# Optimization experiments

Measured on AMD Instinct MI355X. Metric: run time of the kernel, lower is better.

## Reference

```python
import jax, jax.numpy as jnp
import numpy as np

HEADS = 8
DK = 64            # key_size == size_per_head
NEIGHBORS = 3
KSIZE = 1 + 2 * NEIGHBORS  # 7 (rate=1)


def setup_inputs() -> dict:
    key = jax.random.key(0)
    k1, k2, k3, k4 = jax.random.split(key, 4)
    B, HW, S, D = 2, 64, 256, 512
    inputs = jax.random.normal(k1, (B, HW, S, D), dtype=jnp.float32)
    pos_bias = jax.random.normal(k2, (HEADS, S, KSIZE), dtype=jnp.float32)
    W_qkv = jax.random.normal(k3, (D, 3 * HEADS * DK), dtype=jnp.float32) * 0.02
    W_out = jax.random.normal(k4, (HEADS * DK, D), dtype=jnp.float32) * 0.02
    return {"inputs": inputs, "pos_bias": pos_bias, "W_qkv": W_qkv, "W_out": W_out}


def reference(inputs, pos_bias, W_qkv, W_out):
    B, HW, S, D = inputs.shape
    # qkv projection (no bias), split into q, k, v
    qkv = inputs @ W_qkv                                   # [B,HW,S,3*H*DK]
    q, k, v = jnp.split(qkv, 3, axis=-1)
    q = (q / jnp.sqrt(jnp.float32(DK))).reshape(B, HW, S, HEADS, DK)
    k = k.reshape(B, HW, S, HEADS, DK)
    v = v.reshape(B, HW, S, HEADS, DK)

    # zero-pad keys/values along seq (faithful to F.pad with value=0)
    pad = NEIGHBORS
    kp = jnp.pad(k, ((0, 0), (0, 0), (pad, pad), (0, 0), (0, 0)))
    vp = jnp.pad(v, ((0, 0), (0, 0), (pad, pad), (0, 0), (0, 0)))

    # sliding-window gather: window w for query i covers padded positions i..i+KSIZE-1
    idx = jnp.arange(S)[:, None] + jnp.arange(KSIZE)[None, :]  # [S,KSIZE]
    kw = kp[:, :, idx]                                         # [B,HW,S,KSIZE,H,DK]
    vw = vp[:, :, idx]                                         # [B,HW,S,KSIZE,H,DK]

    # scores over the window
    attn = jnp.einsum('bnshd,bnswhd->bnswh', q, kw)            # [B,HW,S,KSIZE,H]
    # additive positional bias: [H,S,KSIZE] -> [S,KSIZE,H] broadcast
    attn = attn + jnp.transpose(pos_bias, (1, 2, 0))[None, None]
    attn = jax.nn.softmax(attn, axis=-2)                       # softmax over window dim

    out = jnp.einsum('bnswh,bnswhd->bnshd', attn, vw)          # [B,HW,S,H,DK]
    out = out.reshape(B, HW, S, HEADS * DK)
    return out @ W_out
```

## Files before the change

kernel.cpp:

```cpp
#include <hip/hip_runtime.h>
#include <hip/hip_bf16.h>
#include <cstdint>


typedef __bf16 bf16x8 __attribute__((ext_vector_type(8)));
typedef float f32x4 __attribute__((ext_vector_type(4)));

__device__ __forceinline__ uint16_t f2bf(float f) {
    uint32_t u = __builtin_bit_cast(uint32_t, f);
    return (uint16_t)((u + 0x7fffu + ((u >> 16) & 1u)) >> 16);
}
__device__ __forceinline__ float bflo(uint32_t u) { return __builtin_bit_cast(float, u << 16); }
__device__ __forceinline__ float bfhi(uint32_t u) { return __builtin_bit_cast(float, u & 0xffff0000u); }

__device__ __forceinline__ void unpack8(uint4 v, float* f) {
    f[0] = bflo(v.x); f[1] = bfhi(v.x);
    f[2] = bflo(v.y); f[3] = bfhi(v.y);
    f[4] = bflo(v.z); f[5] = bfhi(v.z);
    f[6] = bflo(v.w); f[7] = bfhi(v.w);
}
__device__ __forceinline__ uint32_t pack2(float a, float b) {
    return (uint32_t)f2bf(a) | ((uint32_t)f2bf(b) << 16);
}

#define GLOAD_LDS16(gp, lp)                                                        \
    __builtin_amdgcn_global_load_lds((const __attribute__((address_space(1))) void*)(gp), \
                                     (__attribute__((address_space(3))) void*)(lp), 16, 0, 0)

__device__ __forceinline__ bf16x8 ds_read16(const uint16_t* p) {
    bf16x8 r;
    asm volatile("ds_read_b128 %0, %1"
                 : "=v"(r)
                 : "v"((const __attribute__((address_space(3))) void*)p));
    return r;
}

__global__ void prep(const float* __restrict__ X, const float* __restrict__ Wqkv,
                     const float* __restrict__ Wout, uint16_t* __restrict__ Xb,
                     uint16_t* __restrict__ WqkvT, uint16_t* __restrict__ WoutT) {
    int b = blockIdx.x;
    if (b < 8192) {
        int i = b * 256 + threadIdx.x;
        const float4* p = (const float4*)X + (size_t)i * 2;
        float4 a = p[0], q = p[1];
        uint4 o;
        o.x = pack2(a.x, a.y);
        o.y = pack2(a.z, a.w);
        o.z = pack2(q.x, q.y);
        o.w = pack2(q.z, q.w);
        *((uint4*)Xb + i) = o;
    } else {
        int idx = (b - 8192) * 256 + threadIdx.x;
        if (idx < 512 * 1536) {
            int r = idx / 1536, c = idx - r * 1536;
            WqkvT[(size_t)c * 512 + r] = f2bf(Wqkv[idx]);
        } else {
            idx -= 512 * 1536;
            int r = idx >> 9, c = idx & 511;
            WoutT[(size_t)c * 512 + r] = f2bf(Wout[idx]);
        }
    }
}

__global__ __launch_bounds__(512, 2)
void gemm_qkv_attn(const uint16_t* __restrict__ Xb, const uint16_t* __restrict__ WqkvT,
                   const float* __restrict__ pb, uint16_t* __restrict__ attn) {
    __shared__ __align__(16) uint16_t lds[57344];

    constexpr int KO = 16384;
    constexpr int VO = 33152;
    constexpr int PO = 49920;

    const int tid  = threadIdx.x;
    const int lane = tid & 63;
    const int wv   = tid >> 6;
    const int r    = lane & 15;
    const int quad = lane >> 4;
    const int wr   = wv >> 1;
    const int wc   = wv & 1;
    const int h    = blockIdx.x >> 7;
    const int bn   = blockIdx.x & 127;
    const long bm0 = (long)bn * 256;

    const uint16_t* srcp[4];
    int rel[4];
#pragma unroll
    for (int i = 0; i < 4; ++i) {
        int j = wv * 256 + i * 64 + lane;
        if (j < 1024) {
            int d = j, ln = d >> 3, pre = (d & 7) ^ (ln & 7);
            int row = 2 * ln + (pre >> 2), col = (pre & 3) * 8;
            srcp[i] = Xb + (bm0 + row) * 512L + col;
            rel[i]  = d * 8;
        } else {
            int e = j - 1024, ln = e >> 3, pre = (e & 7) ^ (ln & 7);
            int row = 2 * ln + (pre >> 2), col = (pre & 3) * 8;
            long grow = ((long)(row >> 6)) * 512 + h * 64 + (row & 63);
            srcp[i] = WqkvT + grow * 512 + col;
            rel[i]  = e * 8;
        }
    }

#define STAGE(q_, t_) do {                                                              \
        if (wv < 4) {                                                                   \
            _Pragma("unroll")                                                           \
            for (int i_ = 0; i_ < 4; ++i_)                                              \
                GLOAD_LDS16(srcp[i_] + (t_) * 32, &lds[(q_) * 8192 + rel[i_]]);         \
        } else if (wv < 7) {                                                            \
            _Pragma("unroll")                                                           \
            for (int i_ = 0; i_ < 4; ++i_)                                              \
                GLOAD_LDS16(srcp[i_] + (t_) * 32, &lds[32768 + (q_) * 6144 + rel[i_]]); \
        }                                                                               \
    } while (0)

    const int p_ln  = (((r & 1) << 2) | quad) ^ ((r >> 1) & 7);
    const int aLane = wr * 2048 + (r >> 1) * 64 + p_ln * 8;
    const int bLane = wc * 3072 + (r >> 1) * 64 + p_ln * 8;

    f32x4 acc[4][6];
#pragma unroll
    for (int mf = 0; mf < 4; ++mf)
#pragma unroll
        for (int nf = 0; nf < 6; ++nf) acc[mf][nf] = (f32x4){0.f, 0.f, 0.f, 0.f};

    bf16x8 fA0[4], fB0[6], fA1[4], fB1[6];

#define READS(q_, FA_, FB_) do {                                                        \
        const int ao_ = (q_) * 8192, bo_ = 32768 + (q_) * 6144;                         \
        _Pragma("unroll")                                                               \
        for (int nf_ = 0; nf_ < 6; ++nf_) FB_[nf_] = ds_read16(&lds[bo_ + bLane + nf_ * 512]); \
        _Pragma("unroll")                                                               \
        for (int mf_ = 0; mf_ < 4; ++mf_) FA_[mf_] = ds_read16(&lds[ao_ + aLane + mf_ * 512]); \
    } while (0)

#define BODY(t_, FAn_, FBn_, FAc_, FBc_) do {                                           \
        if ((t_) + 1 < 16) {                                                            \
            READS(((t_) + 1) & 3, FAn_, FBn_);                                          \
            asm volatile("s_waitcnt lgkmcnt(10)" ::: "memory");                         \
        } else {                                                                        \
            asm volatile("s_waitcnt lgkmcnt(0)" ::: "memory");                          \
        }                                                                               \
        __builtin_amdgcn_sched_barrier(0);                                              \
        __builtin_amdgcn_s_setprio(1);                                                  \
        _Pragma("unroll")                                                               \
        for (int nf_ = 0; nf_ < 6; ++nf_)                                               \
            _Pragma("unroll")                                                           \
            for (int mf_ = 0; mf_ < 4; ++mf_)                                           \
                acc[mf_][nf_] = __builtin_amdgcn_mfma_f32_16x16x32_bf16(                \
                    FBc_[nf_], FAc_[mf_], acc[mf_][nf_], 0, 0, 0);                      \
        __builtin_amdgcn_s_setprio(0);                                                  \
        if ((t_) + 3 < 16) {                                                            \
            STAGE(((t_) + 3) & 3, (t_) + 3);                                            \
            asm volatile("s_waitcnt vmcnt(4)" ::: "memory");                            \
        } else {                                                                        \
            asm volatile("s_waitcnt vmcnt(0)" ::: "memory");                            \
        }                                                                               \
        if ((t_) < 15) __builtin_amdgcn_s_barrier();                                    \
    } while (0)

    STAGE(0, 0);
    STAGE(1, 1);
    STAGE(2, 2);
    asm volatile("s_waitcnt vmcnt(4)" ::: "memory");
    __builtin_amdgcn_s_barrier();
    READS(0, fA0, fB0);

    for (int tt = 0; tt < 16; tt += 2) {
        BODY(tt,     fA1, fB1, fA0, fB0);
        BODY(tt + 1, fA0, fB0, fA1, fB1);
    }

    asm volatile("s_waitcnt vmcnt(0) lgkmcnt(0)" ::: "memory");
    __builtin_amdgcn_s_barrier();

    if (tid < 96) {
        int a    = tid / 48;
        int rem  = tid - a * 48;
        int hr6  = rem >> 3;
        int c8   = rem & 7;
        int hrow = (hr6 < 3) ? hr6 : (256 + hr6);
        ((uint4*)&lds[a ? VO : KO])[hrow * 8 + c8] = (uint4){0u, 0u, 0u, 0u};
    }

#pragma unroll
    for (int nf = 0; nf < 6; ++nf) {
        int arr, d0;
        if (wc == 0) { if (nf < 4) { arr = 0; d0 = nf * 16; } else { arr = 1; d0 = (nf - 4) * 16; } }
        else         { if (nf < 2) { arr = 1; d0 = 32 + nf * 16; } else { arr = 2; d0 = (nf - 2) * 16; } }
        const int base = (arr == 0) ? 0 : ((arr == 1) ? KO : VO);
        const int hofs = (arr == 0) ? 0 : 3;
        const int cc0  = (d0 >> 3) + (quad >> 1);
        const int sub  = (quad & 1) * 4;
#pragma unroll
        for (int mf = 0; mf < 4; ++mf) {
            int rowX = wr * 64 + mf * 16 + r + hofs;
            uint2 w;
            w.x = pack2(acc[mf][nf][0], acc[mf][nf][1]);
            w.y = pack2(acc[mf][nf][2], acc[mf][nf][3]);
            *(uint2*)&lds[base + rowX * 64 + ((cc0 ^ (rowX & 7)) << 3) + sub] = w;
        }
    }
    __syncthreads();

    const int s     = tid & 255;
    const int half  = tid >> 8;
    const int cbase = half * 4;
    float* pp = (float*)&lds[PO];

    uint4 qc[4];
    const uint4* qarr = (const uint4*)lds;
#pragma unroll
    for (int c = 0; c < 4; ++c) qc[c] = qarr[s * 8 + ((cbase + c) ^ (s & 7))];

    float sc[7];
#pragma unroll
    for (int w = 0; w < 7; ++w) sc[w] = 0.f;
    const uint4* karr = (const uint4*)&lds[KO];
#pragma unroll
    for (int c = 0; c < 4; ++c) {
        float qf[8];
        unpack8(qc[c], qf);
#pragma unroll
        for (int w = 0; w < 7; ++w) {
            int hrow = s + w;
            uint4 kc = karr[hrow * 8 + ((cbase + c) ^ (hrow & 7))];
            float kf[8];
            unpack8(kc, kf);
#pragma unroll
            for (int j = 0; j < 8; ++j) sc[w] += qf[j] * kf[j];
        }
    }

    if (half == 1) {
#pragma unroll
        for (int w = 0; w < 7; ++w) pp[s * 8 + w] = sc[w];
    }
    __syncthreads();

    if (half == 0) {
        const float* pbr = pb + ((size_t)h * 256 + s) * 7;
        float mx = -1e30f, tot[7];
#pragma unroll
        for (int w = 0; w < 7; ++w) {
            tot[w] = (sc[w] + pp[s * 8 + w]) * 0.125f + pbr[w];
            mx = fmaxf(mx, tot[w]);
        }
        float sum = 0.f;
#pragma unroll
        for (int w = 0; w < 7; ++w) {
            tot[w] = __expf(tot[w] - mx);
            sum += tot[w];
        }
        const float inv = 1.f / sum;
#pragma unroll
        for (int w = 0; w < 7; ++w) pp[s * 8 + w] = tot[w] * inv;
    }
    __syncthreads();

    float p[7];
#pragma unroll
    for (int w = 0; w < 7; ++w) p[w] = pp[s * 8 + w];

    const uint4* varr = (const uint4*)&lds[VO];
    uint4 ov[4];
#pragma unroll
    for (int c = 0; c < 4; ++c) {
        float o[8] = {0.f, 0.f, 0.f, 0.f, 0.f, 0.f, 0.f, 0.f};
#pragma unroll
        for (int w = 0; w < 7; ++w) {
            int hrow = s + w;
            uint4 vc = varr[hrow * 8 + ((cbase + c) ^ (hrow & 7))];
            float vf[8];
            unpack8(vc, vf);
#pragma unroll
            for (int j = 0; j < 8; ++j) o[j] += p[w] * vf[j];
        }
        ov[c].x = pack2(o[0], o[1]);
        ov[c].y = pack2(o[2], o[3]);
        ov[c].z = pack2(o[4], o[5]);
        ov[c].w = pack2(o[6], o[7]);
    }
    uint16_t* orow = attn + ((size_t)(bn * 256 + s)) * 512 + h * 64 + cbase * 8;
#pragma unroll
    for (int c = 0; c < 4; ++c) *(uint4*)(orow + c * 8) = ov[c];
#undef STAGE
#undef READS
#undef BODY
}

template <bool F32OUT>
__global__ __launch_bounds__(512, 4)
void gemm_mn(const uint16_t* __restrict__ A, const uint16_t* __restrict__ BT,
             void* __restrict__ Cout, int M, int N, int K) {
    __shared__ __align__(16) uint16_t lds[36864];

    const int tid  = threadIdx.x;
    const int lane = tid & 63;
    const int wv   = tid >> 6;
    const int r    = lane & 15;
    const int quad = lane >> 4;
    const int wr   = wv >> 1;
    const int wc   = wv & 1;
    const long bm0 = (long)blockIdx.x * 256;
    const long bn0 = (long)blockIdx.y * 128;
    const int NT   = K >> 5;

#define SRC_ROWCOL(d_, row_, col_) do {                                                 \
        int ln_ = (d_) >> 3, pre_ = ((d_) & 7) ^ (ln_ & 7);                             \
        row_ = 2 * ln_ + (pre_ >> 2);                                                   \
        col_ = (pre_ & 3) * 8;                                                          \
    } while (0)
    int rA0, cA0, rA1, cA1, rB0, cB0;
    SRC_ROWCOL(tid,       rA0, cA0);
    SRC_ROWCOL(tid + 512, rA1, cA1);
    SRC_ROWCOL(tid,       rB0, cB0);
    const uint16_t* pA0 = A  + (bm0 + rA0) * (long)K + cA0;
    const uint16_t* pA1 = A  + (bm0 + rA1) * (long)K + cA1;
    const uint16_t* pB0 = BT + (bn0 + rB0) * (long)K + cB0;
#undef SRC_ROWCOL

#define STAGE(b_, t_) do {                                                              \
        GLOAD_LDS16(pA0 + (t_) * 32, &lds[(b_) * 8192 + tid * 8]);                      \
        GLOAD_LDS16(pA1 + (t_) * 32, &lds[(b_) * 8192 + (tid + 512) * 8]);              \
        GLOAD_LDS16(pB0 + (t_) * 32, &lds[24576 + (b_) * 4096 + tid * 8]);              \
    } while (0)

    const int p_ln  = (((r & 1) << 2) | quad) ^ ((r >> 1) & 7);
    const int aLane = wr * 2048 + (r >> 1) * 64 + p_ln * 8;
    const int bLane = 24576 + wc * 2048 + (r >> 1) * 64 + p_ln * 8;

#define DS_A(mf_) ds_read16(&lds[aoff + aLane + (mf_) * 512])
#define DS_B(nf_) ds_read16(&lds[boff + bLane + (nf_) * 512])
#define WAITK2 do { asm volatile("s_waitcnt lgkmcnt(2)" ::: "memory");                  \
                    __builtin_amdgcn_sched_barrier(0); } while (0)
#define WAITK0 do { asm volatile("s_waitcnt lgkmcnt(0)" ::: "memory");                  \
                    __builtin_amdgcn_sched_barrier(0); } while (0)
#define MFMA_CL(m0_, f0_, f1_)                                                          \
    __builtin_amdgcn_s_setprio(1);                                                      \
    _Pragma("unroll")                                                                   \
    for (int nf = 0; nf < 4; ++nf)                                                      \
        acc[(m0_)][nf] = __builtin_amdgcn_mfma_f32_16x16x32_bf16(bfr[nf], f0_,          \
                                                                 acc[(m0_)][nf], 0, 0, 0); \
    _Pragma("unroll")                                                                   \
    for (int nf = 0; nf < 4; ++nf)                                                      \
        acc[(m0_) + 1][nf] = __builtin_amdgcn_mfma_f32_16x16x32_bf16(bfr[nf], f1_,      \
                                                                 acc[(m0_) + 1][nf], 0, 0, 0); \
    __builtin_amdgcn_s_setprio(0);

    f32x4 acc[4][4];
#pragma unroll
    for (int mf = 0; mf < 4; ++mf)
#pragma unroll
        for (int nf = 0; nf < 4; ++nf) acc[mf][nf] = (f32x4){0.f, 0.f, 0.f, 0.f};

    STAGE(0, 0);
    STAGE(1, 1);
    asm volatile("s_waitcnt vmcnt(3)" ::: "memory");
    __builtin_amdgcn_s_barrier();

    int b = 0, bs = 2;
    for (int t = 0; t < NT; ++t) {
        const int aoff = b * 8192;
        const int boff = b * 4096;

        if (t + 2 < NT) STAGE(bs, t + 2);

        bf16x8 bfr[4], a0, a1, a2, a3;
#pragma unroll
        for (int nf = 0; nf < 4; ++nf) bfr[nf] = DS_B(nf);
        a0 = DS_A(0); a1 = DS_A(1);
        a2 = DS_A(2); a3 = DS_A(3);

        WAITK2;
        MFMA_CL(0, a0, a1)
        WAITK0;
        MFMA_CL(2, a2, a3)

        if (t + 1 < NT) {
            if (t + 2 < NT)
                asm volatile("s_waitcnt vmcnt(3)" ::: "memory");
            else
                asm volatile("s_waitcnt vmcnt(0)" ::: "memory");
            __builtin_amdgcn_s_barrier();
        }
        b  = (b  == 2) ? 0 : b + 1;
        bs = (bs == 2) ? 0 : bs + 1;
    }

#pragma unroll
    for (int mf = 0; mf < 4; ++mf) {
        long m = bm0 + wr * 64 + mf * 16 + r;
#pragma unroll
        for (int nf = 0; nf < 4; ++nf) {
            long n0 = bn0 + wc * 64 + nf * 16 + quad * 4;
            if (F32OUT) {
                float4 v = {acc[mf][nf][0], acc[mf][nf][1], acc[mf][nf][2], acc[mf][nf][3]};
                *(float4*)((float*)Cout + m * (long)N + n0) = v;
            } else {
                uint2 w;
                w.x = pack2(acc[mf][nf][0], acc[mf][nf][1]);
                w.y = pack2(acc[mf][nf][2], acc[mf][nf][3]);
                *(uint2*)((uint16_t*)Cout + m * (long)N + n0) = w;
            }
        }
    }
#undef STAGE
#undef DS_A
#undef DS_B
#undef WAITK2
#undef WAITK0
#undef MFMA_CL
}

extern "C" void kernel_launch(void* const* d_in, const int* in_sizes, int n_in,
                              void* d_out, int out_size, void* d_ws, size_t ws_size,
                              hipStream_t stream) {
    const float* X    = (const float*)d_in[0];
    const float* pb   = (const float*)d_in[1];
    const float* Wqkv = (const float*)d_in[2];
    const float* Wout = (const float*)d_in[3];
    float* out = (float*)d_out;

    char* ws = (char*)d_ws;
    uint16_t* WqkvT = (uint16_t*)(ws);
    uint16_t* WoutT = (uint16_t*)(ws + 1572864);
    uint16_t* Xb    = (uint16_t*)(ws + 2097152);
    uint16_t* attnb = (uint16_t*)(ws + 35651584);

    prep<<<12288, 256, 0, stream>>>(X, Wqkv, Wout, Xb, WqkvT, WoutT);
    gemm_qkv_attn<<<1024, 512, 0, stream>>>(Xb, WqkvT, pb, attnb);
    gemm_mn<true><<<dim3(128, 4), 512, 0, stream>>>(attnb, WoutT, out, 32768, 512, 512);
}
```

Before: 230.7 us.

## Fuse fp32-to-bf16 conversion of X into the QKV GEMM load path

Drops the separate prep pass that converted X to bf16 in workspace. The QKV+attention kernel now loads fp32 X directly with register loads, packs it to bf16 and writes it into swizzled LDS, while the weights still go through direct global-to-LDS loads. The main pipeline goes from a 4-deep LDS ring to double buffering with full vmcnt/lgkmcnt waits and a barrier every step. This removes the conversion kernel's X write and re-read, but each head's block now reads twice as many bytes of X, and latency hiding in the main loop is shallower.

Result: slower. 241.1 us (+4.5%).

```diff
diff --git a/kernel.cpp b/kernel.cpp
--- a/kernel.cpp
+++ b/kernel.cpp
@@ -5,6 +5,7 @@
 
 typedef __bf16 bf16x8 __attribute__((ext_vector_type(8)));
 typedef float f32x4 __attribute__((ext_vector_type(4)));
+typedef uint32_t u32x4 __attribute__((ext_vector_type(4)));
 
 __device__ __forceinline__ uint16_t f2bf(float f) {
     uint32_t u = __builtin_bit_cast(uint32_t, f);
@@ -34,42 +35,41 @@
                  : "v"((const __attribute__((address_space(3))) void*)p));
     return r;
 }
-
-__global__ void prep(const float* __restrict__ X, const float* __restrict__ Wqkv,
-                     const float* __restrict__ Wout, uint16_t* __restrict__ Xb,
+__device__ __forceinline__ void ds_write16(uint16_t* p, u32x4 w) {
+    asm volatile("ds_write_b128 %0, %1"
+                 :: "v"((__attribute__((address_space(3))) void*)p), "v"(w)
+                 : "memory");
+}
+__device__ __forceinline__ f32x4 gload4f(const float* p) {
+    f32x4 r;
+    asm volatile("global_load_dwordx4 %0, %1, off"
+                 : "=v"(r)
+                 : "v"((const __attribute__((address_space(1))) void*)p));
+    return r;
+}
+
+__global__ void prep(const float* __restrict__ Wqkv, const float* __restrict__ Wout,
                      uint16_t* __restrict__ WqkvT, uint16_t* __restrict__ WoutT) {
-    int b = blockIdx.x;
-    if (b < 8192) {
-        int i = b * 256 + threadIdx.x;
-        const float4* p = (const float4*)X + (size_t)i * 2;
-        float4 a = p[0], q = p[1];
-        uint4 o;
-        o.x = pack2(a.x, a.y);
-        o.y = pack2(a.z, a.w);
-        o.z = pack2(q.x, q.y);
-        o.w = pack2(q.z, q.w);
-        *((uint4*)Xb + i) = o;
+    int idx = blockIdx.x * 256 + threadIdx.x;
+    if (idx < 512 * 1536) {
+        int r = idx / 1536, c = idx - r * 1536;
+        WqkvT[(size_t)c * 512 + r] = f2bf(Wqkv[idx]);
     } else {
-        int idx = (b - 8192) * 256 + threadIdx.x;
-        if (idx < 512 * 1536) {
-            int r = idx / 1536, c = idx - r * 1536;
-            WqkvT[(size_t)c * 512 + r] = f2bf(Wqkv[idx]);
-        } else {
-            idx -= 512 * 1536;
-            int r = idx >> 9, c = idx & 511;
-            WoutT[(size_t)c * 512 + r] = f2bf(Wout[idx]);
-        }
+        idx -= 512 * 1536;
+        int r = idx >> 9, c = idx & 511;
+        WoutT[(size_t)c * 512 + r] = f2bf(Wout[idx]);
     }
 }
 
 __global__ __launch_bounds__(512, 2)
-void gemm_qkv_attn(const uint16_t* __restrict__ Xb, const uint16_t* __restrict__ WqkvT,
+void gemm_qkv_attn(const float* __restrict__ X, const uint16_t* __restrict__ WqkvT,
                    const float* __restrict__ pb, uint16_t* __restrict__ attn) {
-    __shared__ __align__(16) uint16_t lds[57344];
+    __shared__ __align__(16) uint16_t lds[54016];
 
     constexpr int KO = 16384;
     constexpr int VO = 33152;
     constexpr int PO = 49920;
+    constexpr int BB = 16384;
 
     const int tid  = threadIdx.x;
     const int lane = tid & 63;
@@ -82,35 +82,49 @@
     const int bn   = blockIdx.x & 127;
     const long bm0 = (long)bn * 256;
 
-    const uint16_t* srcp[4];
-    int rel[4];
-#pragma unroll
-    for (int i = 0; i < 4; ++i) {
-        int j = wv * 256 + i * 64 + lane;
-        if (j < 1024) {
-            int d = j, ln = d >> 3, pre = (d & 7) ^ (ln & 7);
-            int row = 2 * ln + (pre >> 2), col = (pre & 3) * 8;
-            srcp[i] = Xb + (bm0 + row) * 512L + col;
-            rel[i]  = d * 8;
-        } else {
-            int e = j - 1024, ln = e >> 3, pre = (e & 7) ^ (ln & 7);
-            int row = 2 * ln + (pre >> 2), col = (pre & 3) * 8;
-            long grow = ((long)(row >> 6)) * 512 + h * 64 + (row & 63);
-            srcp[i] = WqkvT + grow * 512 + col;
-            rel[i]  = e * 8;
-        }
-    }
-
-#define STAGE(q_, t_) do {                                                              \
-        if (wv < 4) {                                                                   \
-            _Pragma("unroll")                                                           \
-            for (int i_ = 0; i_ < 4; ++i_)                                              \
-                GLOAD_LDS16(srcp[i_] + (t_) * 32, &lds[(q_) * 8192 + rel[i_]]);         \
-        } else if (wv < 7) {                                                            \
-            _Pragma("unroll")                                                           \
-            for (int i_ = 0; i_ < 4; ++i_)                                              \
-                GLOAD_LDS16(srcp[i_] + (t_) * 32, &lds[32768 + (q_) * 6144 + rel[i_]]); \
-        }                                                                               \
+    const int arow_g = tid >> 1;
+    const int ahalf  = tid & 1;
+    const float* xsrc = X + (bm0 + arow_g) * 512L + ahalf * 16;
+    const int a_ln = arow_g >> 1, a_hr = arow_g & 1;
+    const int c0 = ahalf * 2, c1 = ahalf * 2 + 1;
+    const int ad0 = (a_ln * 8 + ((a_hr * 4 + c0) ^ (a_ln & 7))) * 8;
+    const int ad1 = (a_ln * 8 + ((a_hr * 4 + c1) ^ (a_ln & 7))) * 8;
+
+#define SRC_ROWCOL(d_, row_, col_) do {                                                 \
+        int ln_ = (d_) >> 3, pre_ = ((d_) & 7) ^ (ln_ & 7);                             \
+        row_ = 2 * ln_ + (pre_ >> 2);                                                   \
+        col_ = (pre_ & 3) * 8;                                                          \
+    } while (0)
+    int rB0, cB0, rB1, cB1;
+    SRC_ROWCOL(tid,       rB0, cB0);
+    SRC_ROWCOL(tid + 512, rB1, cB1);
+#undef SRC_ROWCOL
+    const long gB0 = ((long)(rB0 >> 6)) * 512 + h * 64 + (rB0 & 63);
+    const long gB1 = ((long)(rB1 >> 6)) * 512 + h * 64 + (rB1 & 63);
+    const uint16_t* pB0 = WqkvT + gB0 * 512 + cB0;
+    const uint16_t* pB1 = WqkvT + gB1 * 512 + cB1;
+
+#define STAGE_B(qb_, t_) do {                                                           \
+        GLOAD_LDS16(pB0 + (t_) * 32, &lds[BB + (qb_) * 6144 + tid * 8]);                \
+        if (tid < 256)                                                                  \
+            GLOAD_LDS16(pB1 + (t_) * 32, &lds[BB + (qb_) * 6144 + (tid + 512) * 8]);    \
+    } while (0)
+
+    f32x4 ag0, ag1, ag2, ag3;
+#define A_GL(t_) do {                                                                   \
+        const float* p_ = xsrc + (t_) * 32;                                             \
+        ag0 = gload4f(p_);     ag1 = gload4f(p_ + 4);                                   \
+        ag2 = gload4f(p_ + 8); ag3 = gload4f(p_ + 12);                                  \
+    } while (0)
+
+#define PACK_WRITE(x_) do {                                                             \
+        u32x4 w0_, w1_;                                                                 \
+        w0_[0] = pack2(ag0[0], ag0[1]); w0_[1] = pack2(ag0[2], ag0[3]);                 \
+        w0_[2] = pack2(ag1[0], ag1[1]); w0_[3] = pack2(ag1[2], ag1[3]);                 \
+        w1_[0] = pack2(ag2[0], ag2[1]); w1_[1] = pack2(ag2[2], ag2[3]);                 \
+        w1_[2] = pack2(ag3[0], ag3[1]); w1_[3] = pack2(ag3[2], ag3[3]);                 \
+        ds_write16(&lds[((x_) & 1) * 8192 + ad0], w0_);                                 \
+        ds_write16(&lds[((x_) & 1) * 8192 + ad1], w1_);                                 \
     } while (0)
 
     const int p_ln  = (((r & 1) << 2) | quad) ^ ((r >> 1) & 7);
@@ -125,21 +139,25 @@
 
     bf16x8 fA0[4], fB0[6], fA1[4], fB1[6];
 
-#define READS(q_, FA_, FB_) do {                                                        \
-        const int ao_ = (q_) * 8192, bo_ = 32768 + (q_) * 6144;                         \
+#define READS(qb_, FA_, FB_) do {                                                       \
+        const int ao_ = (qb_) * 8192, bo_ = BB + (qb_) * 6144;                          \
         _Pragma("unroll")                                                               \
         for (int nf_ = 0; nf_ < 6; ++nf_) FB_[nf_] = ds_read16(&lds[bo_ + bLane + nf_ * 512]); \
         _Pragma("unroll")                                                               \
         for (int mf_ = 0; mf_ < 4; ++mf_) FA_[mf_] = ds_read16(&lds[ao_ + aLane + mf_ * 512]); \
     } while (0)
 
-#define BODY(t_, FAn_, FBn_, FAc_, FBc_) do {                                           \
-        if ((t_) + 1 < 16) {                                                            \
-            READS(((t_) + 1) & 3, FAn_, FBn_);                                          \
-            asm volatile("s_waitcnt lgkmcnt(10)" ::: "memory");                         \
-        } else {                                                                        \
-            asm volatile("s_waitcnt lgkmcnt(0)" ::: "memory");                          \
+#define BODY(T_, FAc_, FBc_, FAn_, FBn_) do {                                           \
+        if ((T_) + 1 < 16) {                                                            \
+            asm volatile("s_waitcnt vmcnt(0)" ::: "memory");                            \
+            __builtin_amdgcn_sched_barrier(0);                                          \
+            PACK_WRITE((T_) + 1);                                                       \
         }                                                                               \
+        asm volatile("s_waitcnt lgkmcnt(0)" ::: "memory");                              \
+        __builtin_amdgcn_sched_barrier(0);                                              \
+        __builtin_amdgcn_s_barrier();                                                   \
+        if ((T_) + 1 < 16) READS(((T_) + 1) & 1, FAn_, FBn_);                           \
+        if ((T_) + 2 < 16) { STAGE_B((T_) & 1, (T_) + 2); A_GL((T_) + 2); }             \
         __builtin_amdgcn_sched_barrier(0);                                              \
         __builtin_amdgcn_s_setprio(1);                                                  \
         _Pragma("unroll")                                                               \
@@ -149,25 +167,20 @@
                 acc[mf_][nf_] = __builtin_amdgcn_mfma_f32_16x16x32_bf16(                \
                     FBc_[nf_], FAc_[mf_], acc[mf_][nf_], 0, 0, 0);                      \
         __builtin_amdgcn_s_setprio(0);                                                  \
-        if ((t_) + 3 < 16) {                                                            \
-            STAGE(((t_) + 3) & 3, (t_) + 3);                                            \
-            asm volatile("s_waitcnt vmcnt(4)" ::: "memory");                            \
-        } else {                                                                        \
-            asm volatile("s_waitcnt vmcnt(0)" ::: "memory");                            \
-        }                                                                               \
-        if ((t_) < 15) __builtin_amdgcn_s_barrier();                                    \
-    } while (0)
-
-    STAGE(0, 0);
-    STAGE(1, 1);
-    STAGE(2, 2);
-    asm volatile("s_waitcnt vmcnt(4)" ::: "memory");
+    } while (0)
+
+    STAGE_B(0, 0); A_GL(0);
+    asm volatile("s_waitcnt vmcnt(0)" ::: "memory");
+    __builtin_amdgcn_sched_barrier(0);
+    PACK_WRITE(0);
+    STAGE_B(1, 1); A_GL(1);
+    asm volatile("s_waitcnt lgkmcnt(0)" ::: "memory");
     __builtin_amdgcn_s_barrier();
     READS(0, fA0, fB0);
 
     for (int tt = 0; tt < 16; tt += 2) {
-        BODY(tt,     fA1, fB1, fA0, fB0);
-        BODY(tt + 1, fA0, fB0, fA1, fB1);
+        BODY(tt,     fA0, fB0, fA1, fB1);
+        BODY(tt + 1, fA1, fB1, fA0, fB0);
     }
 
     asm volatile("s_waitcnt vmcnt(0) lgkmcnt(0)" ::: "memory");
@@ -283,7 +296,9 @@
     uint16_t* orow = attn + ((size_t)(bn * 256 + s)) * 512 + h * 64 + cbase * 8;
 #pragma unroll
     for (int c = 0; c < 4; ++c) *(uint4*)(orow + c * 8) = ov[c];
-#undef STAGE
+#undef STAGE_B
+#undef A_GL
+#undef PACK_WRITE
 #undef READS
 #undef BODY
 }
@@ -424,10 +439,9 @@
     char* ws = (char*)d_ws;
     uint16_t* WqkvT = (uint16_t*)(ws);
     uint16_t* WoutT = (uint16_t*)(ws + 1572864);
-    uint16_t* Xb    = (uint16_t*)(ws + 2097152);
-    uint16_t* attnb = (uint16_t*)(ws + 35651584);
-
-    prep<<<12288, 256, 0, stream>>>(X, Wqkv, Wout, Xb, WqkvT, WoutT);
-    gemm_qkv_attn<<<1024, 512, 0, stream>>>(Xb, WqkvT, pb, attnb);
+    uint16_t* attnb = (uint16_t*)(ws + 2097152);
+
+    prep<<<4096, 256, 0, stream>>>(Wqkv, Wout, WqkvT, WoutT);
+    gemm_qkv_attn<<<1024, 512, 0, stream>>>(X, WqkvT, pb, attnb);
     gemm_mn<true><<<dim3(128, 4), 512, 0, stream>>>(attnb, WoutT, out, 32768, 512, 512);
 }
```
